# Kernel tuning notes

Hardware: AMD Instinct MI355X
Metric: run time of the kernel (lower is better)

## Reference

```python
import jax, jax.numpy as jnp
import numpy as np
from jax import lax

B, T = 64, 1000
DEC, ENC, ATT, FILT, KS = 1024, 512, 128, 32, 31
PAD = (KS - 1) // 2


def setup_inputs() -> dict:
    key = jax.random.key(0)
    ks = jax.random.split(key, 9)
    return {
        "decoder_hidden": jax.random.normal(ks[0], (B, DEC), dtype=jnp.float32),
        "encoder_outputs": jax.random.normal(ks[1], (B, T, ENC), dtype=jnp.float32),
        "prev_weights": jax.random.uniform(ks[2], (B, T), dtype=jnp.float32),
        "prev_weights_cum": jax.random.uniform(ks[3], (B, T), dtype=jnp.float32),
        "mask": jnp.zeros((B, T), dtype=bool),
        # learned parameters (torch Linear weight layout: [out, in])
        "conv_w": jax.random.normal(ks[4], (FILT, 2, KS), dtype=jnp.float32) * 0.05,
        "loc_proj_w": jax.random.normal(ks[5], (ATT, FILT), dtype=jnp.float32) * 0.05,
        "query_w": jax.random.normal(ks[6], (ATT, DEC), dtype=jnp.float32) * 0.02,
        "key_w": jax.random.normal(ks[7], (ATT, ENC), dtype=jnp.float32) * 0.02,
        "value_w": jax.random.normal(ks[8], (1, ATT), dtype=jnp.float32) * 0.05,
    }


def reference(decoder_hidden, encoder_outputs, prev_weights, prev_weights_cum,
              mask, conv_w, loc_proj_w, query_w, key_w, value_w):
    # query: (B, ATT)
    query = decoder_hidden @ query_w.T
    # keys: (B, T, ATT)
    keys = jnp.einsum('bte,ae->bta', encoder_outputs, key_w)
    # location features: (B, 2, T) -> conv -> (B, FILT, T)
    loc_feats = jnp.stack([prev_weights, prev_weights_cum], axis=1)
    proc_loc = lax.conv_general_dilated(
        loc_feats, conv_w, window_strides=(1,), padding=[(PAD, PAD)],
        dimension_numbers=('NCH', 'OIH', 'NCH'))
    # (B, T, FILT) -> (B, T, ATT)
    proc_loc = jnp.einsum('bft,af->bta', proc_loc, loc_proj_w)
    # energies: (B, T)
    hidden = jnp.tanh(query[:, None, :] + keys + proc_loc)
    energies = jnp.einsum('bta,a->bt', hidden, value_w[0])
    energies = jnp.where(mask, -jnp.inf, energies)
    attention_weights = jax.nn.softmax(energies, axis=1)
    # context: (B, ENC)
    context = jnp.einsum('bt,bte->be', attention_weights, encoder_outputs)
    return context, attention_weights
```

## Files before the change

kernel.cpp:

```cpp
#include <hip/hip_runtime.h>
#include <hip/hip_bf16.h>
#include <math.h>

#define BB   64
#define TT   1000
#define DEC  1024
#define ENCD 512
#define ATT  128
#define FILT 32
#define KSZ  31
#define PADW 15
#define BT   32
#define NTL  32
#define XWN  64

typedef __attribute__((ext_vector_type(8))) short bf16x8;
typedef __attribute__((ext_vector_type(4))) float f32x4;

static __device__ __forceinline__ ushort f2bf(float f) {
    union { float f; unsigned u; } v; v.f = f;
    unsigned r = (v.u + 0x7FFFu + ((v.u >> 16) & 1u)) >> 16;
    return (ushort)r;
}

static __device__ __forceinline__ bf16x8 cvt8(float4 lo, float4 hi) {
    union { __hip_bfloat162 h[4]; bf16x8 v; } u;
    u.h[0] = __float22bfloat162_rn(make_float2(lo.x, lo.y));
    u.h[1] = __float22bfloat162_rn(make_float2(lo.z, lo.w));
    u.h[2] = __float22bfloat162_rn(make_float2(hi.x, hi.y));
    u.h[3] = __float22bfloat162_rn(make_float2(hi.z, hi.w));
    return u.v;
}

static __device__ __forceinline__ float fast_tanh(float x) {
    float e = __expf(2.f * x);
    return 1.f - 2.f * __builtin_amdgcn_rcpf(e + 1.f);
}

static __device__ __forceinline__ void gl2lds16(const void* g, void* l) {
    __builtin_amdgcn_global_load_lds(
        (const __attribute__((address_space(1))) unsigned*)g,
        (__attribute__((address_space(3))) unsigned*)l, 16, 0, 0);
}

__global__ __launch_bounds__(256) void k_prep(const float* __restrict__ kw,
                                              const float* __restrict__ cw,
                                              const float* __restrict__ lpw,
                                              const float* __restrict__ dh,
                                              const float* __restrict__ qw,
                                              const float* __restrict__ vw,
                                              ushort* __restrict__ kwbF,
                                              float* __restrict__ q,
                                              float* __restrict__ Mbuf) {
    __shared__ float qred[128];
    if (blockIdx.x < 32) {
        int idx = blockIdx.x * 256 + threadIdx.x;
        int l  = idx & 63;
        int n  = (idx >> 6) & 7;
        int ks = (idx >> 9) & 1;
        int c  = idx >> 10;
        int a  = n * 16 + (l & 15);
        int k0 = c * 64 + ks * 32 + (l >> 4) * 8;
        ushort u[8];
        #pragma unroll
        for (int j = 0; j < 8; ++j) u[j] = f2bf(kw[a * ENCD + k0 + j]);
        *(uint4*)&kwbF[(size_t)idx * 8] = *(const uint4*)u;
    } else if (blockIdx.x < 36) {
        int idx = (blockIdx.x - 32) * 256 + threadIdx.x;
        int l  = idx & 63;
        int n  = (idx >> 6) & 7;
        int ks = (idx >> 9) & 1;
        int a  = n * 16 + (l & 15);
        int s  = l >> 4;
        ushort u[8];
        #pragma unroll
        for (int j = 0; j < 8; ++j) {
            int k = s * 8 + j;
            float v = 0.f;
            if (k < KSZ) {
                #pragma unroll
                for (int f = 0; f < FILT; ++f)
                    v += cw[(f * 2 + ks) * KSZ + k] * lpw[a * FILT + f];
            }
            u[j] = f2bf(v);
        }
        *(uint4*)&kwbF[(size_t)(((16 + ks) * 8 + n) * 64 + l) * 8] = *(const uint4*)u;
    } else if (blockIdx.x == 36) {
        if (threadIdx.x < 64) {
            float m0 = fabsf(vw[threadIdx.x]) + fabsf(vw[threadIdx.x + 64]);
            #pragma unroll
            for (int off = 1; off < 64; off <<= 1) m0 += __shfl_xor(m0, off, 64);
            if (threadIdx.x == 0) Mbuf[0] = m0;
        }
    } else {
        int b  = blockIdx.x - 37;
        int a  = threadIdx.x & 127;
        int kh = threadIdx.x >> 7;
        const float* dhb = dh + b * DEC + kh * 512;
        const float* qwa = qw + a * DEC + kh * 512;
        float s = 0.f;
        #pragma unroll 4
        for (int k = 0; k < 512; k += 4) {
            float4 x = *(const float4*)&dhb[k];
            float4 w = *(const float4*)&qwa[k];
            s += x.x * w.x + x.y * w.y + x.z * w.z + x.w * w.w;
        }
        if (kh == 1) qred[a] = s;
        __syncthreads();
        if (kh == 0) q[b * ATT + a] = s + qred[a];
    }
}

__global__ __launch_bounds__(256) void k_energies(
    const float* __restrict__ enc, const float* __restrict__ pw,
    const float* __restrict__ pwc, const unsigned char* __restrict__ mask,
    const ushort* __restrict__ kwbF, const float* __restrict__ vw,
    const float* __restrict__ q, const float* __restrict__ Mbuf,
    float* __restrict__ expE, float* __restrict__ pctx,
    float* __restrict__ ps)
{
    __shared__ __align__(16) float As[BT * ENCD];
    __shared__ __align__(16) float xw[2][XWN];
    __shared__ float pequad[4][BT];
    __shared__ float sExp[BT];

    const int b    = blockIdx.x;
    const int tile = blockIdx.y;
    const int t0   = tile * BT;
    const int tid  = threadIdx.x;
    const int w    = tid >> 6;
    const int l    = tid & 63;
    const int r    = l & 15;
    const int sl   = l >> 4;

    const float* encb = enc + (size_t)b * TT * ENCD;

    for (int i = tid; i < 2 * XWN; i += 256) {
        int c  = i / XWN;
        int ii = i - c * XWN;
        int tg = t0 + ii - PADW;
        const float* src = c ? pwc : pw;
        xw[c][ii] = (ii < BT + KSZ - 1 && tg >= 0 && tg < TT) ? src[b * TT + tg] : 0.f;
    }
    __builtin_amdgcn_sched_barrier(0);

    #pragma unroll
    for (int j = 0; j < 8; ++j) {
        int rl = w * 8 + j;
        int rg = t0 + rl; if (rg >= TT) rg = TT - 1;
        const float* src = encb + (size_t)rg * ENCD + (size_t)(sl * 16 + (r ^ (rl & 15))) * 4;
        gl2lds16(src, (char*)As + rl * 2048);
    }
    __builtin_amdgcn_sched_barrier(0);

    uint4 bA[2][2], bB[2][2], bC[2][2], bD[2][2], bW[2][2];
    auto loadB = [&](uint4 (&dst)[2][2], int c) {
        #pragma unroll
        for (int ks = 0; ks < 2; ++ks)
            #pragma unroll
            for (int nn = 0; nn < 2; ++nn)
                dst[ks][nn] = *(const uint4*)&kwbF[(size_t)(((c * 2 + ks) * 8 + w * 2 + nn) * 64 + l) * 8];
    };
    loadB(bA, 0); loadB(bB, 1); loadB(bC, 2); loadB(bD, 3); loadB(bW, 8);
    __builtin_amdgcn_sched_barrier(0);

    #pragma unroll
    for (int j = 0; j < 8; ++j) {
        int rl = w * 8 + j;
        int rg = t0 + rl; if (rg >= TT) rg = TT - 1;
        const float* src = encb + (size_t)rg * ENCD + 256 + (size_t)(sl * 16 + (r ^ (rl & 15))) * 4;
        gl2lds16(src, (char*)As + rl * 2048 + 1024);
    }
    __builtin_amdgcn_sched_barrier(0);
    asm volatile("s_waitcnt vmcnt(8) lgkmcnt(0)" ::: "memory");
    __builtin_amdgcn_sched_barrier(0);
    __builtin_amdgcn_s_barrier();

    f32x4 acc[2][2];
    #pragma unroll
    for (int i = 0; i < 2; ++i)
        #pragma unroll
        for (int n = 0; n < 2; ++n) acc[i][n] = (f32x4){0.f, 0.f, 0.f, 0.f};

    auto compute = [&](int c, const uint4 (&bfr)[2][2]) {
        #pragma unroll
        for (int ks = 0; ks < 2; ++ks) {
            const int u = ks * 8 + sl * 2;
            bf16x8 af[2];
            #pragma unroll
            for (int i = 0; i < 2; ++i) {
                int row = i * 16 + r;
                const char* base = (const char*)As + row * 2048 + c * 256;
                float4 alo = *(const float4*)(base + ((u ^ (row & 15)) << 4));
                float4 ahi = *(const float4*)(base + (((u + 1) ^ (row & 15)) << 4));
                af[i] = cvt8(alo, ahi);
            }
            __builtin_amdgcn_s_setprio(1);
            #pragma unroll
            for (int i = 0; i < 2; ++i)
                #pragma unroll
                for (int nn = 0; nn < 2; ++nn)
                    acc[i][nn] = __builtin_amdgcn_mfma_f32_16x16x32_bf16(
                        af[i], *(const bf16x8*)&bfr[ks][nn], acc[i][nn], 0, 0, 0);
            __builtin_amdgcn_s_setprio(0);
        }
    };
    auto computeFeat = [&](const uint4 (&bfr)[2][2]) {
        #pragma unroll
        for (int ks = 0; ks < 2; ++ks) {
            bf16x8 af[2];
            #pragma unroll
            for (int i = 0; i < 2; ++i) {
                int row = i * 16 + r;
                const float* xp = &xw[ks][row + sl * 8];
                af[i] = cvt8(make_float4(xp[0], xp[1], xp[2], xp[3]),
                             make_float4(xp[4], xp[5], xp[6], xp[7]));
            }
            __builtin_amdgcn_s_setprio(1);
            #pragma unroll
            for (int i = 0; i < 2; ++i)
                #pragma unroll
                for (int nn = 0; nn < 2; ++nn)
                    acc[i][nn] = __builtin_amdgcn_mfma_f32_16x16x32_bf16(
                        af[i], *(const bf16x8*)&bfr[ks][nn], acc[i][nn], 0, 0, 0);
            __builtin_amdgcn_s_setprio(0);
        }
    };

    compute(0, bA); compute(1, bB); compute(2, bC); compute(3, bD);
    computeFeat(bW);

    asm volatile("s_waitcnt vmcnt(0)" ::: "memory");
    __builtin_amdgcn_sched_barrier(0);
    __builtin_amdgcn_s_barrier();

    loadB(bA, 4); loadB(bB, 5); loadB(bC, 6); loadB(bD, 7);
    compute(4, bA); compute(5, bB); compute(6, bC); compute(7, bD);

    const float* qb = q + b * ATT;
    const float M = Mbuf[0];
    float pe[2][4];
    #pragma unroll
    for (int i = 0; i < 2; ++i)
        #pragma unroll
        for (int rr = 0; rr < 4; ++rr) pe[i][rr] = 0.f;
    #pragma unroll
    for (int nn = 0; nn < 2; ++nn) {
        int a = w * 32 + nn * 16 + r;
        float vvn = vw[a];
        float qvn = qb[a];
        #pragma unroll
        for (int i = 0; i < 2; ++i)
            #pragma unroll
            for (int rr = 0; rr < 4; ++rr)
                pe[i][rr] += vvn * fast_tanh(acc[i][nn][rr] + qvn);
    }
    #pragma unroll
    for (int m = 1; m < 16; m <<= 1)
        #pragma unroll
        for (int i = 0; i < 2; ++i)
            #pragma unroll
            for (int rr = 0; rr < 4; ++rr)
                pe[i][rr] += __shfl_xor(pe[i][rr], m, 64);
    if (r == 0) {
        #pragma unroll
        for (int i = 0; i < 2; ++i)
            #pragma unroll
            for (int rr = 0; rr < 4; ++rr)
                pequad[w][i * 16 + sl * 4 + rr] = pe[i][rr];
    }
    __syncthreads();
    if (tid < BT) {
        int t = t0 + tid;
        float e = pequad[0][tid] + pequad[1][tid] + pequad[2][tid] + pequad[3][tid];
        float v = 0.f;
        if (t < TT && !mask[b * TT + t]) v = __expf(e - M);
        if (t < TT) expE[b * TT + t] = v;
        sExp[tid] = v;
        float sv = v;
        #pragma unroll
        for (int off = 1; off < 32; off <<= 1) sv += __shfl_xor(sv, off, 64);
        if (tid == 0) ps[b * NTL + tile] = sv;
    }
    __syncthreads();

    {
        const int U   = tid >> 1;
        const int sub = (tid & 1) * 8;
        float2 cacc = make_float2(0.f, 0.f);
        #pragma unroll 4
        for (int t = 0; t < BT; ++t) {
            float s = sExp[t];
            int byte = t * 2048 + (((U & ~15) | ((U ^ (t & 15)) & 15)) << 4) + sub;
            float2 v = *(const float2*)((const char*)As + byte);
            cacc.x += s * v.x; cacc.y += s * v.y;
        }
        *(float2*)&pctx[(size_t)(b * NTL + tile) * ENCD + tid * 2] = cacc;
    }
}

__global__ __launch_bounds__(256) void k_ctx_reduce(const float* __restrict__ pctx,
                                                    const float* __restrict__ ps,
                                                    const float* __restrict__ expE,
                                                    float* __restrict__ ctx,
                                                    float* __restrict__ wout) {
    int bid = blockIdx.x, tid = threadIdx.x;
    __shared__ float sps[NTL];
    int b = (bid < BB) ? bid : (bid - BB);
    if (tid < NTL) sps[tid] = ps[b * NTL + tid];
    __syncthreads();
    float s = 0.f;
    #pragma unroll
    for (int i = 0; i < NTL; ++i) s += sps[i];
    float inv = 1.f / s;
    if (bid < BB) {
        float2 a = make_float2(0.f, 0.f);
        #pragma unroll
        for (int i = 0; i < NTL; ++i) {
            float2 v = *(const float2*)&pctx[(size_t)(b * NTL + i) * ENCD + tid * 2];
            a.x += v.x; a.y += v.y;
        }
        a.x *= inv; a.y *= inv;
        *(float2*)&ctx[b * ENCD + tid * 2] = a;
    } else {
        for (int t = tid; t < TT; t += 256)
            wout[b * TT + t] = expE[b * TT + t] * inv;
    }
}

extern "C" void kernel_launch(void* const* d_in, const int* in_sizes, int n_in,
                              void* d_out, int out_size, void* d_ws, size_t ws_size,
                              hipStream_t stream) {
    const float* dh   = (const float*)d_in[0];
    const float* enc  = (const float*)d_in[1];
    const float* pw   = (const float*)d_in[2];
    const float* pwc  = (const float*)d_in[3];
    const unsigned char* mask = (const unsigned char*)d_in[4];
    const float* cw   = (const float*)d_in[5];
    const float* lpw  = (const float*)d_in[6];
    const float* qw   = (const float*)d_in[7];
    const float* kw   = (const float*)d_in[8];
    const float* vw   = (const float*)d_in[9];

    float* out_ctx = (float*)d_out;
    float* out_w   = out_ctx + BB * ENCD;

    float* wsf    = (float*)d_ws;
    float*  q     = wsf;
    float*  expE  = wsf + 8192;
    float*  ps    = wsf + 8192 + 64000;
    float*  pctx  = wsf + 8192 + 64000 + 2048;
    ushort* kwbF  = (ushort*)(wsf + 8192 + 64000 + 2048 + 1048576);
    float*  Mbuf  = wsf + 8192 + 64000 + 2048 + 1048576 + 36864;

    k_prep    <<<dim3(101),     dim3(256), 0, stream>>>(kw, cw, lpw, dh, qw, vw, kwbF, q, Mbuf);
    k_energies<<<dim3(BB, NTL), dim3(256), 0, stream>>>(enc, pw, pwc, mask, kwbF, vw, q, Mbuf, expE, pctx, ps);
    k_ctx_reduce <<<dim3(128),  dim3(256), 0, stream>>>(pctx, ps, expE, out_ctx, out_w);
}
```

Measured before the change: 63.90 us.

## Halve time tile to 16 rows to double energy-kernel blocks; batch query GEMV

Shrinks the time tile of the energies kernel from 32 to 16 rows, so 63 tiles per batch replace 32. This doubles the grid for more parallelism and lighter per-block LDS use and register pressure. Each wave now issues one MFMA row group instead of two, and weight fragments are reloaded per block, so the share of fixed overhead rises. The query GEMV in the prep kernel is also restructured so each block computes four batch rows over the full K, dropping the shared-memory reduction and cutting the prep grid. The ctx reduce now sums twice as many partials.

```diff
diff --git a/kernel.cpp b/kernel.cpp
--- a/kernel.cpp
+++ b/kernel.cpp
@@ -10,9 +10,9 @@
 #define FILT 32
 #define KSZ  31
 #define PADW 15
-#define BT   32
-#define NTL  32
-#define XWN  64
+#define BT   16
+#define NTL  63
+#define XWN  48
 
 typedef __attribute__((ext_vector_type(8))) short bf16x8;
 typedef __attribute__((ext_vector_type(4))) float f32x4;
@@ -52,7 +52,6 @@
                                               ushort* __restrict__ kwbF,
                                               float* __restrict__ q,
                                               float* __restrict__ Mbuf) {
-    __shared__ float qred[128];
     if (blockIdx.x < 32) {
         int idx = blockIdx.x * 256 + threadIdx.x;
         int l  = idx & 63;
@@ -93,21 +92,23 @@
             if (threadIdx.x == 0) Mbuf[0] = m0;
         }
     } else {
-        int b  = blockIdx.x - 37;
+        int b0 = (blockIdx.x - 37) * 4;
         int a  = threadIdx.x & 127;
-        int kh = threadIdx.x >> 7;
-        const float* dhb = dh + b * DEC + kh * 512;
-        const float* qwa = qw + a * DEC + kh * 512;
-        float s = 0.f;
-        #pragma unroll 4
-        for (int k = 0; k < 512; k += 4) {
-            float4 x = *(const float4*)&dhb[k];
-            float4 w = *(const float4*)&qwa[k];
-            s += x.x * w.x + x.y * w.y + x.z * w.z + x.w * w.w;
-        }
-        if (kh == 1) qred[a] = s;
-        __syncthreads();
-        if (kh == 0) q[b * ATT + a] = s + qred[a];
+        int bh = threadIdx.x >> 7;
+        const float* qwa = qw + a * DEC;
+        #pragma unroll
+        for (int p = 0; p < 2; ++p) {
+            int b = b0 + p * 2 + bh;
+            const float* dhb = dh + b * DEC;
+            float s = 0.f;
+            #pragma unroll 4
+            for (int k = 0; k < DEC; k += 4) {
+                float4 x = *(const float4*)&dhb[k];
+                float4 w = *(const float4*)&qwa[k];
+                s += x.x * w.x + x.y * w.y + x.z * w.z + x.w * w.w;
+            }
+            q[b * ATT + a] = s;
+        }
     }
 }
 
@@ -135,9 +136,9 @@
 
     const float* encb = enc + (size_t)b * TT * ENCD;
 
-    for (int i = tid; i < 2 * XWN; i += 256) {
-        int c  = i / XWN;
-        int ii = i - c * XWN;
+    if (tid < 2 * XWN) {
+        int c  = tid / XWN;
+        int ii = tid - c * XWN;
         int tg = t0 + ii - PADW;
         const float* src = c ? pwc : pw;
         xw[c][ii] = (ii < BT + KSZ - 1 && tg >= 0 && tg < TT) ? src[b * TT + tg] : 0.f;
@@ -145,8 +146,8 @@
     __builtin_amdgcn_sched_barrier(0);
 
     #pragma unroll
-    for (int j = 0; j < 8; ++j) {
-        int rl = w * 8 + j;
+    for (int j = 0; j < 4; ++j) {
+        int rl = w * 4 + j;
         int rg = t0 + rl; if (rg >= TT) rg = TT - 1;
         const float* src = encb + (size_t)rg * ENCD + (size_t)(sl * 16 + (r ^ (rl & 15))) * 4;
         gl2lds16(src, (char*)As + rl * 2048);
@@ -165,64 +166,48 @@
     __builtin_amdgcn_sched_barrier(0);
 
     #pragma unroll
-    for (int j = 0; j < 8; ++j) {
-        int rl = w * 8 + j;
+    for (int j = 0; j < 4; ++j) {
+        int rl = w * 4 + j;
         int rg = t0 + rl; if (rg >= TT) rg = TT - 1;
         const float* src = encb + (size_t)rg * ENCD + 256 + (size_t)(sl * 16 + (r ^ (rl & 15))) * 4;
         gl2lds16(src, (char*)As + rl * 2048 + 1024);
     }
     __builtin_amdgcn_sched_barrier(0);
-    asm volatile("s_waitcnt vmcnt(8) lgkmcnt(0)" ::: "memory");
+    asm volatile("s_waitcnt vmcnt(4) lgkmcnt(0)" ::: "memory");
     __builtin_amdgcn_sched_barrier(0);
     __builtin_amdgcn_s_barrier();
 
-    f32x4 acc[2][2];
-    #pragma unroll
-    for (int i = 0; i < 2; ++i)
-        #pragma unroll
-        for (int n = 0; n < 2; ++n) acc[i][n] = (f32x4){0.f, 0.f, 0.f, 0.f};
+    f32x4 acc[2];
+    acc[0] = (f32x4){0.f, 0.f, 0.f, 0.f};
+    acc[1] = (f32x4){0.f, 0.f, 0.f, 0.f};
 
     auto compute = [&](int c, const uint4 (&bfr)[2][2]) {
         #pragma unroll
         for (int ks = 0; ks < 2; ++ks) {
             const int u = ks * 8 + sl * 2;
-            bf16x8 af[2];
-            #pragma unroll
-            for (int i = 0; i < 2; ++i) {
-                int row = i * 16 + r;
-                const char* base = (const char*)As + row * 2048 + c * 256;
-                float4 alo = *(const float4*)(base + ((u ^ (row & 15)) << 4));
-                float4 ahi = *(const float4*)(base + (((u + 1) ^ (row & 15)) << 4));
-                af[i] = cvt8(alo, ahi);
-            }
+            const char* base = (const char*)As + r * 2048 + c * 256;
+            float4 alo = *(const float4*)(base + ((u ^ r) << 4));
+            float4 ahi = *(const float4*)(base + (((u + 1) ^ r) << 4));
+            bf16x8 af = cvt8(alo, ahi);
             __builtin_amdgcn_s_setprio(1);
             #pragma unroll
-            for (int i = 0; i < 2; ++i)
-                #pragma unroll
-                for (int nn = 0; nn < 2; ++nn)
-                    acc[i][nn] = __builtin_amdgcn_mfma_f32_16x16x32_bf16(
-                        af[i], *(const bf16x8*)&bfr[ks][nn], acc[i][nn], 0, 0, 0);
+            for (int nn = 0; nn < 2; ++nn)
+                acc[nn] = __builtin_amdgcn_mfma_f32_16x16x32_bf16(
+                    af, *(const bf16x8*)&bfr[ks][nn], acc[nn], 0, 0, 0);
             __builtin_amdgcn_s_setprio(0);
         }
     };
     auto computeFeat = [&](const uint4 (&bfr)[2][2]) {
         #pragma unroll
         for (int ks = 0; ks < 2; ++ks) {
-            bf16x8 af[2];
-            #pragma unroll
-            for (int i = 0; i < 2; ++i) {
-                int row = i * 16 + r;
-                const float* xp = &xw[ks][row + sl * 8];
-                af[i] = cvt8(make_float4(xp[0], xp[1], xp[2], xp[3]),
+            const float* xp = &xw[ks][r + sl * 8];
+            bf16x8 af = cvt8(make_float4(xp[0], xp[1], xp[2], xp[3]),
                              make_float4(xp[4], xp[5], xp[6], xp[7]));
-            }
             __builtin_amdgcn_s_setprio(1);
             #pragma unroll
-            for (int i = 0; i < 2; ++i)
-                #pragma unroll
-                for (int nn = 0; nn < 2; ++nn)
-                    acc[i][nn] = __builtin_amdgcn_mfma_f32_16x16x32_bf16(
-                        af[i], *(const bf16x8*)&bfr[ks][nn], acc[i][nn], 0, 0, 0);
+            for (int nn = 0; nn < 2; ++nn)
+                acc[nn] = __builtin_amdgcn_mfma_f32_16x16x32_bf16(
+                    af, *(const bf16x8*)&bfr[ks][nn], acc[nn], 0, 0, 0);
             __builtin_amdgcn_s_setprio(0);
         }
     };
@@ -239,35 +224,27 @@
 
     const float* qb = q + b * ATT;
     const float M = Mbuf[0];
-    float pe[2][4];
-    #pragma unroll
-    for (int i = 0; i < 2; ++i)
-        #pragma unroll
-        for (int rr = 0; rr < 4; ++rr) pe[i][rr] = 0.f;
+    float pe[4];
+    #pragma unroll
+    for (int rr = 0; rr < 4; ++rr) pe[rr] = 0.f;
     #pragma unroll
     for (int nn = 0; nn < 2; ++nn) {
         int a = w * 32 + nn * 16 + r;
         float vvn = vw[a];
         float qvn = qb[a];
         #pragma unroll
-        for (int i = 0; i < 2; ++i)
-            #pragma unroll
-            for (int rr = 0; rr < 4; ++rr)
-                pe[i][rr] += vvn * fast_tanh(acc[i][nn][rr] + qvn);
+        for (int rr = 0; rr < 4; ++rr)
+            pe[rr] += vvn * fast_tanh(acc[nn][rr] + qvn);
     }
     #pragma unroll
     for (int m = 1; m < 16; m <<= 1)
         #pragma unroll
-        for (int i = 0; i < 2; ++i)
-            #pragma unroll
-            for (int rr = 0; rr < 4; ++rr)
-                pe[i][rr] += __shfl_xor(pe[i][rr], m, 64);
+        for (int rr = 0; rr < 4; ++rr)
+            pe[rr] += __shfl_xor(pe[rr], m, 64);
     if (r == 0) {
         #pragma unroll
-        for (int i = 0; i < 2; ++i)
-            #pragma unroll
-            for (int rr = 0; rr < 4; ++rr)
-                pequad[w][i * 16 + sl * 4 + rr] = pe[i][rr];
+        for (int rr = 0; rr < 4; ++rr)
+            pequad[w][sl * 4 + rr] = pe[rr];
     }
     __syncthreads();
     if (tid < BT) {
@@ -279,7 +256,7 @@
         sExp[tid] = v;
         float sv = v;
         #pragma unroll
-        for (int off = 1; off < 32; off <<= 1) sv += __shfl_xor(sv, off, 64);
+        for (int off = 1; off < 16; off <<= 1) sv += __shfl_xor(sv, off, 64);
         if (tid == 0) ps[b * NTL + tile] = sv;
     }
     __syncthreads();
@@ -315,7 +292,6 @@
     float inv = 1.f / s;
     if (bid < BB) {
         float2 a = make_float2(0.f, 0.f);
-        #pragma unroll
         for (int i = 0; i < NTL; ++i) {
             float2 v = *(const float2*)&pctx[(size_t)(b * NTL + i) * ENCD + tid * 2];
             a.x += v.x; a.y += v.y;
@@ -349,11 +325,11 @@
     float*  q     = wsf;
     float*  expE  = wsf + 8192;
     float*  ps    = wsf + 8192 + 64000;
-    float*  pctx  = wsf + 8192 + 64000 + 2048;
-    ushort* kwbF  = (ushort*)(wsf + 8192 + 64000 + 2048 + 1048576);
-    float*  Mbuf  = wsf + 8192 + 64000 + 2048 + 1048576 + 36864;
-
-    k_prep    <<<dim3(101),     dim3(256), 0, stream>>>(kw, cw, lpw, dh, qw, vw, kwbF, q, Mbuf);
+    float*  pctx  = wsf + 8192 + 64000 + 4096;
+    ushort* kwbF  = (ushort*)(wsf + 8192 + 64000 + 4096 + 2064384);
+    float*  Mbuf  = wsf + 8192 + 64000 + 4096 + 2064384 + 36864;
+
+    k_prep    <<<dim3(53),      dim3(256), 0, stream>>>(kw, cw, lpw, dh, qw, vw, kwbF, q, Mbuf);
     k_energies<<<dim3(BB, NTL), dim3(256), 0, stream>>>(enc, pw, pwc, mask, kwbF, vw, q, Mbuf, expE, pctx, ps);
     k_ctx_reduce <<<dim3(128),  dim3(256), 0, stream>>>(pctx, ps, expE, out_ctx, out_w);
 }
```

New measurement: 114.7 us. 1.79x slower.
